# Performance work log

Hardware: AMD Instinct MI355X
Metric: run time of the kernel (lower is better)

Reference implementation:

```python
import jax, jax.numpy as jnp
import numpy as np

B, TK, NK, H = 64, 512, 256, 512

def _masked_renorm_softmax(scores, mask):
    # softmax over last dim, multiply by mask, renormalize (as in the torch code)
    p = jax.nn.softmax(scores, axis=-1) * mask
    return p / jnp.sum(p, axis=-1, keepdims=True)

def setup_inputs() -> dict:
    key = jax.random.key(0)
    ks = jax.random.split(key, 14)
    s = 0.02
    return {
        "s_t_hat": jax.random.normal(ks[0], (B, 2 * H), jnp.float32),
        "encoder_outputs_token": jax.random.normal(ks[1], (B, TK, H), jnp.float32),
        "encoder_outputs_node": jax.random.normal(ks[2], (B, NK, H), jnp.float32),
        "node_to_token": jax.random.randint(ks[3], (B, TK), 0, NK),
        "enc_padding_mask_token": jnp.ones((B, TK), jnp.float32),
        "enc_padding_mask_node": jnp.ones((B, NK), jnp.float32),
        "graph": jax.random.uniform(ks[4], (B, NK, NK), jnp.float32),
        "flow": jax.random.uniform(ks[5], (B, NK), jnp.float32),
        # parameters (Linear weights stored as [in, out]; x @ W == torch Linear)
        "W_c": jax.random.normal(ks[6], (H,), jnp.float32) * s,          # Linear(1, H)
        "W_tok": jax.random.normal(ks[7], (H, H), jnp.float32) * s,      # encode_proj_token
        "W_node": jax.random.normal(ks[8], (H, H), jnp.float32) * s,     # encode_proj_node
        "W_dec": jax.random.normal(ks[9], (2 * H, H), jnp.float32) * s,  # decode_proj
        "b_dec": jnp.zeros((H,), jnp.float32),
        "v_tok": jax.random.normal(ks[10], (H,), jnp.float32) * s,       # v_token
        "v_node": jax.random.normal(ks[11], (H,), jnp.float32) * s,      # v_node
    }

def reference(s_t_hat, encoder_outputs_token, encoder_outputs_node, node_to_token,
              enc_padding_mask_token, enc_padding_mask_node, graph, flow,
              W_c, W_tok, W_node, W_dec, b_dec, v_tok, v_node):
    # projections
    enc_tok_feat = jnp.einsum('bth,hk->btk', encoder_outputs_token, W_tok)   # [B,TK,H]
    enc_node_feat = jnp.einsum('bnh,hk->bnk', encoder_outputs_node, W_node)  # [B,NK,H]
    dec_fea = s_t_hat @ W_dec + b_dec                                        # [B,H]
    flow_feat = flow[..., None] * W_c                                        # [B,NK,H]

    # node attention
    e_node = jnp.tanh(enc_node_feat + dec_fea[:, None, :] + flow_feat)
    scores_node = jnp.einsum('bnh,h->bn', e_node, v_node)                    # [B,NK]
    attn_dist_node = _masked_renorm_softmax(scores_node, enc_padding_mask_node)

    # gather node attention onto tokens via node_to_token indices
    gathered = jnp.take_along_axis(attn_dist_node, node_to_token, axis=1)    # [B,TK]
    attn_dist_node_to_token = _masked_renorm_softmax(gathered, enc_padding_mask_token)

    # token attention
    e_tok = jnp.tanh(enc_tok_feat + dec_fea[:, None, :])
    scores_tok = jnp.einsum('bth,h->bt', e_tok, v_tok)                       # [B,TK]
    attn_dist_token = _masked_renorm_softmax(scores_tok, enc_padding_mask_token)

    # mix and context
    final_attn = 0.5 * attn_dist_token + 0.5 * attn_dist_node_to_token      # [B,TK]
    c_t = jnp.einsum('bt,bth->bh', final_attn, encoder_outputs_token)        # [B,H]

    # multi-hop graph diffusion of node attention
    zero_hop = attn_dist_node                                                # [B,NK]
    one_hop = jnp.einsum('bn,bnm->bm', zero_hop, graph)
    two_hop = jnp.einsum('bn,bnm->bm', one_hop, graph)
    flow_out = (zero_hop + one_hop + two_hop) * 0.33333

    return (c_t, final_attn, attn_dist_node, flow_out)
```

## Files before the change

kernel.cpp:

```cpp
#include <hip/hip_runtime.h>
#include <math.h>

constexpr int kB = 64;
constexpr int kTK = 512;
constexpr int kNK = 256;
constexpr int kH = 512;
constexpr int kTokBlocks = kB * kTK / 64;
constexpr int kNodeBlocks = kB * kNK / 64;

typedef float f32x4 __attribute__((ext_vector_type(4)));
typedef __bf16 bf16x8 __attribute__((ext_vector_type(8)));

__device__ __forceinline__ unsigned short f32_to_bf16(float f) {
  return (unsigned short)((__float_as_uint(f) + 0x8000u) >> 16);
}

__device__ __forceinline__ float tanh_fast(float x) {
  float e = __builtin_amdgcn_exp2f(x * 2.8853900817779268f);
  return 1.0f - 2.0f * __builtin_amdgcn_rcpf(e + 1.0f);
}

__device__ __forceinline__ void lds_barrier() {
  __builtin_amdgcn_s_waitcnt(0xC07F);
  __builtin_amdgcn_s_barrier();
}

__global__ __launch_bounds__(256) void prep_kernel(
    const float* __restrict__ Wtok, const float* __restrict__ Wnode,
    unsigned short* __restrict__ WtokT, unsigned short* __restrict__ WnodeT,
    const float* __restrict__ s_t_hat, const float* __restrict__ W_dec,
    float* __restrict__ dec_part) {
  __shared__ float sm[32 * 33];
  const int tid = threadIdx.x;
  if (blockIdx.x < 512) {
    const int idx = blockIdx.x;
    const int z = idx >> 8, rem = idx & 255;
    const int bx = rem & 15, by = rem >> 4;
    const float* W = z ? Wnode : Wtok;
    unsigned short* T = z ? WnodeT : WtokT;
    const int tx = tid & 31, ty = tid >> 5;
#pragma unroll
    for (int i = 0; i < 4; ++i)
      sm[(ty + 8 * i) * 33 + tx] =
          W[(size_t)(by * 32 + ty + 8 * i) * kH + bx * 32 + tx];
    __syncthreads();
#pragma unroll
    for (int i = 0; i < 4; ++i)
      T[(size_t)(bx * 32 + ty + 8 * i) * kH + by * 32 + tx] =
          f32_to_bf16(sm[tx * 33 + ty + 8 * i]);
  } else {
    const int r = blockIdx.x - 512;
    const int b = r >> 3, s = r & 7;
    if (tid < 128) sm[tid] = s_t_hat[(size_t)b * 1024 + s * 128 + tid];
    __syncthreads();
    float a0 = 0.f, a1 = 0.f;
    const float* w = W_dec + (size_t)(s * 128) * kH;
#pragma unroll 8
    for (int k = 0; k < 128; ++k) {
      a0 = fmaf(sm[k], w[(size_t)k * kH + tid], a0);
      a1 = fmaf(sm[k], w[(size_t)k * kH + tid + 256], a1);
    }
    dec_part[(size_t)(b * 8 + s) * kH + tid] = a0;
    dec_part[(size_t)(b * 8 + s) * kH + tid + 256] = a1;
  }
}

__global__ __launch_bounds__(1024, 4) void scores_fused_kernel(
    const float* __restrict__ enc_tok, const float* __restrict__ enc_node,
    const unsigned short* __restrict__ WtokT,
    const unsigned short* __restrict__ WnodeT,
    const float* __restrict__ dec_part, const float* __restrict__ b_dec,
    const float* __restrict__ flow, const float* __restrict__ W_c,
    const float* __restrict__ v_tok, const float* __restrict__ v_node,
    float* __restrict__ scores_tok, float* __restrict__ scores_node) {
  const int tid = threadIdx.x;
  const int wave = tid >> 6, lane = tid & 63;
  const int quad = lane >> 4, l15 = lane & 15;
  const bool is_node = blockIdx.x >= kTokBlocks;
  const int bidx = is_node ? (int)blockIdx.x - kTokBlocks : (int)blockIdx.x;
  const float* A = is_node ? enc_node : enc_tok;
  const unsigned short* WT = is_node ? WnodeT : WtokT;
  const float* v = is_node ? v_node : v_tok;
  float* scores = is_node ? scores_node : scores_tok;
  const int ROWS = is_node ? kNK : kTK;
  const int b = is_node ? (bidx >> 2) : (bidx >> 3);
  const int row0 = (is_node ? (bidx & 3) : (bidx & 7)) * 64;

  __shared__ __align__(16) unsigned short As[2][8192];
  __shared__ float red[16][64];

  const f32x4 fzero = {0.f, 0.f, 0.f, 0.f};
  f32x4 acc[4][2];
#pragma unroll
  for (int i = 0; i < 4; ++i)
#pragma unroll
    for (int j = 0; j < 2; ++j) acc[i][j] = fzero;

  const int r = tid >> 4;
  const int kcol = tid & 15;
  const float* aptr = A + (size_t)(b * ROWS + row0 + r) * kH + kcol * 4;
  const int k0 = kcol * 4;
  const int k1 = 64 + kcol * 4;
  const int addr0 = (((k0 >> 5) * 4 + (r >> 4)) * 64 + ((k0 >> 3) & 3) * 16 +
                     (r & 15)) * 8 + (k0 & 7);
  const int addr1 = (((k1 >> 5) * 4 + (r >> 4)) * 64 + ((k1 >> 3) & 3) * 16 +
                     (r & 15)) * 8 + (k1 & 7);
  float4 ax0, ax1;
  auto aload = [&](int kc) {
    ax0 = *(const float4*)(aptr + kc * 128);
    ax1 = *(const float4*)(aptr + kc * 128 + 64);
  };
  auto acommit = [&](int buf) {
    ushort4 h0, h1;
    h0.x = f32_to_bf16(ax0.x); h0.y = f32_to_bf16(ax0.y);
    h0.z = f32_to_bf16(ax0.z); h0.w = f32_to_bf16(ax0.w);
    h1.x = f32_to_bf16(ax1.x); h1.y = f32_to_bf16(ax1.y);
    h1.z = f32_to_bf16(ax1.z); h1.w = f32_to_bf16(ax1.w);
    *(ushort4*)&As[buf][addr0] = h0;
    *(ushort4*)&As[buf][addr1] = h1;
  };

  const int n0 = wave * 32;
  const unsigned short* bbase = WT + (size_t)(n0 + l15) * kH + quad * 8;
  bf16x8 bbuf[2][2];
  auto loadB = [&](int sb, int g) {
    bbuf[sb][0] = *(const bf16x8*)(bbase + g * 32);
    bbuf[sb][1] = *(const bf16x8*)(bbase + (size_t)16 * kH + g * 32);
  };

  aload(0);
  acommit(0);
  aload(1);
  loadB(0, 0);
  lds_barrier();

#pragma unroll
  for (int g = 0; g < 16; ++g) {
    const int kc = g >> 2, kh = g & 3;
    if (kh == 0 && kc < 3) {
      acommit((kc + 1) & 1);
      if (kc < 2) aload(kc + 2);
    }
    if (g < 15) loadB((g + 1) & 1, g + 1);
    bf16x8 afr[4];
#pragma unroll
    for (int mi = 0; mi < 4; ++mi)
      afr[mi] = *(const bf16x8*)&As[kc & 1][((kh * 4 + mi) * 64 + lane) * 8];
#pragma unroll
    for (int mi = 0; mi < 4; ++mi)
#pragma unroll
      for (int ni = 0; ni < 2; ++ni)
        acc[mi][ni] = __builtin_amdgcn_mfma_f32_16x16x32_bf16(
            afr[mi], bbuf[g & 1][ni], acc[mi][ni], 0, 0, 0);
    if (kh == 3 && kc < 3) lds_barrier();
  }

  float dec2[2], vv2[2], wc2[2];
#pragma unroll
  for (int ni = 0; ni < 2; ++ni) {
    const int col = n0 + 16 * ni + l15;
    float d = b_dec[col];
#pragma unroll
    for (int p = 0; p < 8; ++p) d += dec_part[(size_t)(b * 8 + p) * kH + col];
    dec2[ni] = d;
    vv2[ni] = v[col];
    wc2[ni] = is_node ? W_c[col] : 0.f;
  }
#pragma unroll
  for (int mi = 0; mi < 4; ++mi) {
#pragma unroll
    for (int reg = 0; reg < 4; ++reg) {
      const int row = 16 * mi + quad * 4 + reg;
      const float fl = is_node ? flow[b * kNK + row0 + row] : 0.f;
      float p = 0.f;
#pragma unroll
      for (int ni = 0; ni < 2; ++ni)
        p += tanh_fast(fmaf(fl, wc2[ni], acc[mi][ni][reg] + dec2[ni])) * vv2[ni];
#pragma unroll
      for (int off = 1; off < 16; off <<= 1) p += __shfl_xor(p, off, 64);
      if (l15 == 0) red[wave][row] = p;
    }
  }
  __syncthreads();
  if (tid < 64) {
    float s = 0.f;
#pragma unroll
    for (int w = 0; w < 16; ++w) s += red[w][tid];
    scores[b * ROWS + row0 + tid] = s;
  }
}

__device__ __forceinline__ float block_sum_512(float v, float* rbuf) {
#pragma unroll
  for (int off = 32; off >= 1; off >>= 1) v += __shfl_xor(v, off, 64);
  if ((threadIdx.x & 63) == 0) rbuf[threadIdx.x >> 6] = v;
  __syncthreads();
  float s = rbuf[0];
#pragma unroll
  for (int w = 1; w < 8; ++w) s += rbuf[w];
  __syncthreads();
  return s;
}

__global__ __launch_bounds__(512) void softmax_mix_kernel(
    const float* __restrict__ scores_node, const float* __restrict__ scores_tok,
    const int* __restrict__ node_to_token,
    const float* __restrict__ mask_tok, const float* __restrict__ mask_node,
    float* __restrict__ out_final, float* __restrict__ out_attn_node,
    float* __restrict__ out_flow) {
  const int b = blockIdx.x, tid = threadIdx.x;
  __shared__ float an_sh[kNK];
  __shared__ float rbuf[8];

  if (tid < kNK) out_flow[b * kNK + tid] = 0.f;

  float en = 0.f;
  if (tid < kNK)
    en = expf(scores_node[b * kNK + tid]) * mask_node[b * kNK + tid];
  float sn = block_sum_512(en, rbuf);
  float an = en / sn;
  if (tid < kNK) {
    an_sh[tid] = an;
    out_attn_node[b * kNK + tid] = an;
  }
  __syncthreads();

  const float mt = mask_tok[b * kTK + tid];
  const int idx = node_to_token[b * kTK + tid];
  float eg = expf(an_sh[idx]) * mt;
  float sg = block_sum_512(eg, rbuf);
  float an2t = eg / sg;

  float et = expf(scores_tok[b * kTK + tid]) * mt;
  float st = block_sum_512(et, rbuf);
  float at = et / st;

  out_final[b * kTK + tid] = 0.5f * (at + an2t);
}

__global__ __launch_bounds__(512) void ct_flow1_kernel(
    const float* __restrict__ final_attn, const float* __restrict__ enc_tok,
    const float* __restrict__ attn_node, const float* __restrict__ graph,
    float* __restrict__ ctp, float* __restrict__ fp1) {
  const int tid = threadIdx.x;
  if (blockIdx.x < 128) {
    const int b = blockIdx.x >> 1, s = blockIdx.x & 1;
    __shared__ float fa[256];
    if (tid < 256) fa[tid] = final_attn[b * kTK + s * 256 + tid];
    __syncthreads();
    const int h4 = (tid & 127) * 4, tsub = tid >> 7;
    float4 acc = {0.f, 0.f, 0.f, 0.f};
    const float* base =
        enc_tok + ((size_t)(b * kTK + s * 256 + tsub * 64)) * kH + h4;
#pragma unroll 8
    for (int t = 0; t < 64; ++t) {
      float4 e = *(const float4*)(base + (size_t)t * kH);
      const float w = fa[tsub * 64 + t];
      acc.x = fmaf(w, e.x, acc.x); acc.y = fmaf(w, e.y, acc.y);
      acc.z = fmaf(w, e.z, acc.z); acc.w = fmaf(w, e.w, acc.w);
    }
    *(float4*)&ctp[((size_t)(b * 8 + s * 4 + tsub)) * kH + h4] = acc;
  } else {
    const int rr = blockIdx.x - 128;
    const int b = rr >> 2, sl = rr & 3;
    __shared__ float z[64];
    __shared__ float part[8][256];
    if (tid < 64) z[tid] = attn_node[b * kNK + sl * 64 + tid];
    __syncthreads();
    const int m4 = (tid & 63) * 4, nsub = tid >> 6;
    float4 acc = {0.f, 0.f, 0.f, 0.f};
    const float* g =
        graph + ((size_t)(b * kNK + sl * 64 + nsub * 8)) * kNK + m4;
#pragma unroll
    for (int n = 0; n < 8; ++n) {
      float4 gg = *(const float4*)(g + (size_t)n * kNK);
      const float w = z[nsub * 8 + n];
      acc.x = fmaf(w, gg.x, acc.x); acc.y = fmaf(w, gg.y, acc.y);
      acc.z = fmaf(w, gg.z, acc.z); acc.w = fmaf(w, gg.w, acc.w);
    }
    *(float4*)&part[nsub][m4] = acc;
    __syncthreads();
    if (tid < 64) {
      float4 s0 = {0.f, 0.f, 0.f, 0.f};
#pragma unroll
      for (int p = 0; p < 8; ++p) {
        float4 pp = *(const float4*)&part[p][tid * 4];
        s0.x += pp.x; s0.y += pp.y; s0.z += pp.z; s0.w += pp.w;
      }
      *(float4*)&fp1[((size_t)(b * 4 + sl)) * kNK + tid * 4] = s0;
    }
  }
}

__global__ __launch_bounds__(512) void ct_flow2_kernel(
    const float* __restrict__ ctp, const float* __restrict__ fp1,
    const float* __restrict__ attn_node, const float* __restrict__ graph,
    float* __restrict__ out_ct, float* __restrict__ out_flow) {
  const int tid = threadIdx.x;
  if (blockIdx.x < 64) {
    const int b = blockIdx.x;
    __shared__ float acc_sh[4][512];
    const int h4 = (tid & 127) * 4, part = tid >> 7;
    float4 a = {0.f, 0.f, 0.f, 0.f};
#pragma unroll
    for (int j = 0; j < 2; ++j) {
      float4 c = *(const float4*)&ctp[((size_t)(b * 8 + part * 2 + j)) * kH + h4];
      a.x += c.x; a.y += c.y; a.z += c.z; a.w += c.w;
    }
    *(float4*)&acc_sh[part][h4] = a;
    __syncthreads();
    if (tid < 128) {
      float4 s = {0.f, 0.f, 0.f, 0.f};
#pragma unroll
      for (int p = 0; p < 4; ++p) {
        float4 pp = *(const float4*)&acc_sh[p][tid * 4];
        s.x += pp.x; s.y += pp.y; s.z += pp.z; s.w += pp.w;
      }
      *(float4*)&out_ct[b * kH + tid * 4] = s;
    }
  } else {
    const int rr = blockIdx.x - 64;
    const int b = rr >> 2, sl = rr & 3;
    __shared__ float one_sh[64];
    __shared__ float part2[8][256];
    if (tid < 64) {
      const int n = sl * 64 + tid;
      float one = 0.f;
#pragma unroll
      for (int p = 0; p < 4; ++p) one += fp1[((size_t)(b * 4 + p)) * kNK + n];
      one_sh[tid] = one;
      atomicAdd(&out_flow[b * kNK + n],
                (attn_node[b * kNK + n] + one) * 0.33333f);
    }
    __syncthreads();
    const int m4 = (tid & 63) * 4, nsub = tid >> 6;
    float4 acc = {0.f, 0.f, 0.f, 0.f};
    const float* g =
        graph + ((size_t)(b * kNK + sl * 64 + nsub * 8)) * kNK + m4;
#pragma unroll
    for (int n = 0; n < 8; ++n) {
      float4 gg = *(const float4*)(g + (size_t)n * kNK);
      const float w = one_sh[sl * 0 + nsub * 8 + n];
      acc.x = fmaf(w, gg.x, acc.x); acc.y = fmaf(w, gg.y, acc.y);
      acc.z = fmaf(w, gg.z, acc.z); acc.w = fmaf(w, gg.w, acc.w);
    }
    *(float4*)&part2[nsub][m4] = acc;
    __syncthreads();
    if (tid < 64) {
      float4 s = {0.f, 0.f, 0.f, 0.f};
#pragma unroll
      for (int p = 0; p < 8; ++p) {
        float4 pp = *(const float4*)&part2[p][tid * 4];
        s.x += pp.x; s.y += pp.y; s.z += pp.z; s.w += pp.w;
      }
      float* dst = &out_flow[b * kNK + tid * 4];
      atomicAdd(dst + 0, s.x * 0.33333f);
      atomicAdd(dst + 1, s.y * 0.33333f);
      atomicAdd(dst + 2, s.z * 0.33333f);
      atomicAdd(dst + 3, s.w * 0.33333f);
    }
  }
}

extern "C" void kernel_launch(void* const* d_in, const int* in_sizes, int n_in,
                              void* d_out, int out_size, void* d_ws, size_t ws_size,
                              hipStream_t stream) {
  (void)in_sizes; (void)n_in; (void)out_size; (void)ws_size;
  const float* s_t_hat  = (const float*)d_in[0];
  const float* enc_tok  = (const float*)d_in[1];
  const float* enc_node = (const float*)d_in[2];
  const int*   n2t      = (const int*)d_in[3];
  const float* mask_tok = (const float*)d_in[4];
  const float* mask_nd  = (const float*)d_in[5];
  const float* graph    = (const float*)d_in[6];
  const float* flow     = (const float*)d_in[7];
  const float* W_c      = (const float*)d_in[8];
  const float* W_tok    = (const float*)d_in[9];
  const float* W_node   = (const float*)d_in[10];
  const float* W_dec    = (const float*)d_in[11];
  const float* b_dec    = (const float*)d_in[12];
  const float* v_tok    = (const float*)d_in[13];
  const float* v_node   = (const float*)d_in[14];

  float* out = (float*)d_out;
  float* out_ct        = out;
  float* out_final     = out + kB * kH;
  float* out_attn_node = out + 2 * kB * kH;
  float* out_flow      = out_attn_node + kB * kNK;

  float* ws = (float*)d_ws;
  float* scores_tok  = ws;
  float* scores_node = ws + 32768;
  float* dec_part    = ws + 49152;
  float* ctp         = dec_part;
  float* fp1         = ws + 311296;
  unsigned short* WtokT  = (unsigned short*)(ws + 376832);
  unsigned short* WnodeT = WtokT + kH * kH;

  prep_kernel<<<1024, 256, 0, stream>>>(W_tok, W_node, WtokT, WnodeT,
                                        s_t_hat, W_dec, dec_part);
  scores_fused_kernel<<<kTokBlocks + kNodeBlocks, 1024, 0, stream>>>(
      enc_tok, enc_node, WtokT, WnodeT, dec_part, b_dec, flow, W_c,
      v_tok, v_node, scores_tok, scores_node);
  softmax_mix_kernel<<<kB, 512, 0, stream>>>(scores_node, scores_tok, n2t,
                                             mask_tok, mask_nd, out_final,
                                             out_attn_node, out_flow);
  ct_flow1_kernel<<<384, 512, 0, stream>>>(out_final, enc_tok, out_attn_node,
                                           graph, ctp, fp1);
  ct_flow2_kernel<<<320, 512, 0, stream>>>(ctp, fp1, out_attn_node, graph,
                                           out_ct, out_flow);
}
```

Baseline: 241.8 us.

## Retile scores GEMM to 128x128 blocks with async LDS B staging and atomics

Replaces the 1024-thread, 64-row by full-N scores kernel with 256-thread blocks computing 128x128 output tiles. The B operand is now staged into LDS through global_load_lds with an XOR swizzle instead of being loaded directly into registers. Because N is split across four column blocks, per-row partial scores are combined with atomicAdd, so prep_kernel now zeroes the score buffers. The larger tiles are meant to improve operand reuse and occupancy, at the cost of atomic contention and a single-buffered A/B pipeline with extra barriers.

Result: slower. 255.9 us (+5.8%).

```diff
diff --git a/kernel.cpp b/kernel.cpp
--- a/kernel.cpp
+++ b/kernel.cpp
@@ -5,11 +5,12 @@
 constexpr int kTK = 512;
 constexpr int kNK = 256;
 constexpr int kH = 512;
-constexpr int kTokBlocks = kB * kTK / 64;
-constexpr int kNodeBlocks = kB * kNK / 64;
+constexpr int kTokGemmBlocks = 256 * 4;
+constexpr int kNodeGemmBlocks = 128 * 4;
 
 typedef float f32x4 __attribute__((ext_vector_type(4)));
 typedef __bf16 bf16x8 __attribute__((ext_vector_type(8)));
+typedef unsigned short u16x8 __attribute__((ext_vector_type(8)));
 
 __device__ __forceinline__ unsigned short f32_to_bf16(float f) {
   return (unsigned short)((__float_as_uint(f) + 0x8000u) >> 16);
@@ -23,13 +24,19 @@
 __device__ __forceinline__ void lds_barrier() {
   __builtin_amdgcn_s_waitcnt(0xC07F);
   __builtin_amdgcn_s_barrier();
+}
+
+__device__ __forceinline__ void async_copy16(void* lds, const void* g) {
+  __builtin_amdgcn_global_load_lds(
+      (const __attribute__((address_space(1))) unsigned int*)g,
+      (__attribute__((address_space(3))) unsigned int*)lds, 16, 0, 0);
 }
 
 __global__ __launch_bounds__(256) void prep_kernel(
     const float* __restrict__ Wtok, const float* __restrict__ Wnode,
     unsigned short* __restrict__ WtokT, unsigned short* __restrict__ WnodeT,
     const float* __restrict__ s_t_hat, const float* __restrict__ W_dec,
-    float* __restrict__ dec_part) {
+    float* __restrict__ dec_part, float* __restrict__ scores_base) {
   __shared__ float sm[32 * 33];
   const int tid = threadIdx.x;
   if (blockIdx.x < 512) {
@@ -50,6 +57,8 @@
           f32_to_bf16(sm[tx * 33 + ty + 8 * i]);
   } else {
     const int r = blockIdx.x - 512;
+    const int tg = r * 256 + tid;
+    if (tg < kB * (kTK + kNK)) scores_base[tg] = 0.f;
     const int b = r >> 3, s = r & 7;
     if (tid < 128) sm[tid] = s_t_hat[(size_t)b * 1024 + s * 128 + tid];
     __syncthreads();
@@ -65,7 +74,7 @@
   }
 }
 
-__global__ __launch_bounds__(1024, 4) void scores_fused_kernel(
+__global__ __launch_bounds__(256, 3) void scores_mfma_kernel(
     const float* __restrict__ enc_tok, const float* __restrict__ enc_node,
     const unsigned short* __restrict__ WtokT,
     const unsigned short* __restrict__ WnodeT,
@@ -76,117 +85,128 @@
   const int tid = threadIdx.x;
   const int wave = tid >> 6, lane = tid & 63;
   const int quad = lane >> 4, l15 = lane & 15;
-  const bool is_node = blockIdx.x >= kTokBlocks;
-  const int bidx = is_node ? (int)blockIdx.x - kTokBlocks : (int)blockIdx.x;
+  const bool is_node = blockIdx.x >= kTokGemmBlocks;
+  const int idx = is_node ? (int)blockIdx.x - kTokGemmBlocks : (int)blockIdx.x;
+  const int rowblk = idx >> 2, colblk = idx & 3;
   const float* A = is_node ? enc_node : enc_tok;
   const unsigned short* WT = is_node ? WnodeT : WtokT;
   const float* v = is_node ? v_node : v_tok;
   float* scores = is_node ? scores_node : scores_tok;
-  const int ROWS = is_node ? kNK : kTK;
-  const int b = is_node ? (bidx >> 2) : (bidx >> 3);
-  const int row0 = (is_node ? (bidx & 3) : (bidx & 7)) * 64;
-
-  __shared__ __align__(16) unsigned short As[2][8192];
-  __shared__ float red[16][64];
+  const int grow0 = rowblk * 128;
+  const int bn = colblk * 128;
+
+  __shared__ __align__(16) unsigned short As[8192];
+  __shared__ __align__(16) unsigned short Bs[8192];
 
   const f32x4 fzero = {0.f, 0.f, 0.f, 0.f};
-  f32x4 acc[4][2];
+  f32x4 acc[4][4];
 #pragma unroll
   for (int i = 0; i < 4; ++i)
 #pragma unroll
-    for (int j = 0; j < 2; ++j) acc[i][j] = fzero;
-
-  const int r = tid >> 4;
-  const int kcol = tid & 15;
-  const float* aptr = A + (size_t)(b * ROWS + row0 + r) * kH + kcol * 4;
-  const int k0 = kcol * 4;
-  const int k1 = 64 + kcol * 4;
-  const int addr0 = (((k0 >> 5) * 4 + (r >> 4)) * 64 + ((k0 >> 3) & 3) * 16 +
-                     (r & 15)) * 8 + (k0 & 7);
-  const int addr1 = (((k1 >> 5) * 4 + (r >> 4)) * 64 + ((k1 >> 3) & 3) * 16 +
-                     (r & 15)) * 8 + (k1 & 7);
-  float4 ax0, ax1;
+    for (int j = 0; j < 4; ++j) acc[i][j] = fzero;
+
+  const int arow = tid >> 1, ahalf = tid & 1;
+  const float* aptr = A + (size_t)(grow0 + arow) * kH + ahalf * 32;
+  float4 ap[8];
   auto aload = [&](int kc) {
-    ax0 = *(const float4*)(aptr + kc * 128);
-    ax1 = *(const float4*)(aptr + kc * 128 + 64);
+#pragma unroll
+    for (int i = 0; i < 8; ++i)
+      ap[i] = *(const float4*)(aptr + kc * 64 + i * 4);
   };
-  auto acommit = [&](int buf) {
-    ushort4 h0, h1;
-    h0.x = f32_to_bf16(ax0.x); h0.y = f32_to_bf16(ax0.y);
-    h0.z = f32_to_bf16(ax0.z); h0.w = f32_to_bf16(ax0.w);
-    h1.x = f32_to_bf16(ax1.x); h1.y = f32_to_bf16(ax1.y);
-    h1.z = f32_to_bf16(ax1.z); h1.w = f32_to_bf16(ax1.w);
-    *(ushort4*)&As[buf][addr0] = h0;
-    *(ushort4*)&As[buf][addr1] = h1;
+  const int fbase = (ahalf * 8 + (arow >> 4)) * 512;
+  const int lbase = (arow & 15) * 8;
+  auto acommit = [&]() {
+#pragma unroll
+    for (int q2 = 0; q2 < 4; ++q2) {
+      u16x8 h;
+      h[0] = f32_to_bf16(ap[q2 * 2].x); h[1] = f32_to_bf16(ap[q2 * 2].y);
+      h[2] = f32_to_bf16(ap[q2 * 2].z); h[3] = f32_to_bf16(ap[q2 * 2].w);
+      h[4] = f32_to_bf16(ap[q2 * 2 + 1].x); h[5] = f32_to_bf16(ap[q2 * 2 + 1].y);
+      h[6] = f32_to_bf16(ap[q2 * 2 + 1].z); h[7] = f32_to_bf16(ap[q2 * 2 + 1].w);
+      *(u16x8*)&As[fbase + q2 * 128 + lbase] = h;
+    }
   };
 
-  const int n0 = wave * 32;
-  const unsigned short* bbase = WT + (size_t)(n0 + l15) * kH + quad * 8;
-  bf16x8 bbuf[2][2];
-  auto loadB = [&](int sb, int g) {
-    bbuf[sb][0] = *(const bf16x8*)(bbase + g * 32);
-    bbuf[sb][1] = *(const bf16x8*)(bbase + (size_t)16 * kH + g * 32);
+  const int nr8 = tid >> 3, kslot = tid & 7;
+  auto stageB = [&](int kc) {
+#pragma unroll
+    for (int j = 0; j < 4; ++j) {
+      const int nrow = j * 32 + nr8;
+      const unsigned short* g =
+          WT + (size_t)(bn + nrow) * kH + kc * 64 + ((kslot ^ (nrow & 7)) * 8);
+      async_copy16(&Bs[j * 2048 + wave * 512], g);
+    }
   };
 
+  const int wm = (wave >> 1) * 4;
+  const int wn = (wave & 1) * 64;
+  auto compute = [&]() {
+#pragma unroll
+    for (int kh = 0; kh < 2; ++kh) {
+      bf16x8 afr[4], bfr[4];
+#pragma unroll
+      for (int mi = 0; mi < 4; ++mi)
+        afr[mi] = *(const bf16x8*)&As[(kh * 8 + wm + mi) * 512 + lane * 8];
+#pragma unroll
+      for (int ni = 0; ni < 4; ++ni) {
+        const int nl = wn + ni * 16 + l15;
+        const int s = kh * 4 + quad;
+        bfr[ni] = *(const bf16x8*)&Bs[nl * 64 + ((s ^ (nl & 7)) * 8)];
+      }
+#pragma unroll
+      for (int mi = 0; mi < 4; ++mi)
+#pragma unroll
+        for (int ni = 0; ni < 4; ++ni)
+          acc[mi][ni] = __builtin_amdgcn_mfma_f32_16x16x32_bf16(
+              afr[mi], bfr[ni], acc[mi][ni], 0, 0, 0);
+    }
+  };
+
   aload(0);
-  acommit(0);
+  acommit();
+  stageB(0);
   aload(1);
-  loadB(0, 0);
-  lds_barrier();
-
-#pragma unroll
-  for (int g = 0; g < 16; ++g) {
-    const int kc = g >> 2, kh = g & 3;
-    if (kh == 0 && kc < 3) {
-      acommit((kc + 1) & 1);
-      if (kc < 2) aload(kc + 2);
-    }
-    if (g < 15) loadB((g + 1) & 1, g + 1);
-    bf16x8 afr[4];
-#pragma unroll
-    for (int mi = 0; mi < 4; ++mi)
-      afr[mi] = *(const bf16x8*)&As[kc & 1][((kh * 4 + mi) * 64 + lane) * 8];
-#pragma unroll
-    for (int mi = 0; mi < 4; ++mi)
-#pragma unroll
-      for (int ni = 0; ni < 2; ++ni)
-        acc[mi][ni] = __builtin_amdgcn_mfma_f32_16x16x32_bf16(
-            afr[mi], bbuf[g & 1][ni], acc[mi][ni], 0, 0, 0);
-    if (kh == 3 && kc < 3) lds_barrier();
-  }
-
-  float dec2[2], vv2[2], wc2[2];
-#pragma unroll
-  for (int ni = 0; ni < 2; ++ni) {
-    const int col = n0 + 16 * ni + l15;
+  __syncthreads();
+
+#pragma unroll 1
+  for (int kc = 0; kc < 8; ++kc) {
+    compute();
+    if (kc < 7) {
+      lds_barrier();
+      acommit();
+      stageB(kc + 1);
+      if (kc < 6) aload(kc + 2);
+      __syncthreads();
+    }
+  }
+
+  const int bb = is_node ? (grow0 >> 8) : (grow0 >> 9);
+  float dec4[4], vv4[4], wc4[4];
+#pragma unroll
+  for (int ni = 0; ni < 4; ++ni) {
+    const int col = bn + wn + ni * 16 + l15;
     float d = b_dec[col];
 #pragma unroll
-    for (int p = 0; p < 8; ++p) d += dec_part[(size_t)(b * 8 + p) * kH + col];
-    dec2[ni] = d;
-    vv2[ni] = v[col];
-    wc2[ni] = is_node ? W_c[col] : 0.f;
-  }
+    for (int p = 0; p < 8; ++p) d += dec_part[(size_t)(bb * 8 + p) * kH + col];
+    dec4[ni] = d;
+    vv4[ni] = v[col];
+    wc4[ni] = is_node ? W_c[col] : 0.f;
+  }
+  const int rbase = grow0 + (wave >> 1) * 64;
 #pragma unroll
   for (int mi = 0; mi < 4; ++mi) {
 #pragma unroll
     for (int reg = 0; reg < 4; ++reg) {
-      const int row = 16 * mi + quad * 4 + reg;
-      const float fl = is_node ? flow[b * kNK + row0 + row] : 0.f;
+      const int row = rbase + 16 * mi + quad * 4 + reg;
+      const float fl = is_node ? flow[row] : 0.f;
       float p = 0.f;
 #pragma unroll
-      for (int ni = 0; ni < 2; ++ni)
-        p += tanh_fast(fmaf(fl, wc2[ni], acc[mi][ni][reg] + dec2[ni])) * vv2[ni];
+      for (int ni = 0; ni < 4; ++ni)
+        p += tanh_fast(fmaf(fl, wc4[ni], acc[mi][ni][reg] + dec4[ni])) * vv4[ni];
 #pragma unroll
       for (int off = 1; off < 16; off <<= 1) p += __shfl_xor(p, off, 64);
-      if (l15 == 0) red[wave][row] = p;
-    }
-  }
-  __syncthreads();
-  if (tid < 64) {
-    float s = 0.f;
-#pragma unroll
-    for (int w = 0; w < 16; ++w) s += red[w][tid];
-    scores[b * ROWS + row0 + tid] = s;
+      if (l15 == 0) atomicAdd(&scores[row], p);
+    }
   }
 }
 
@@ -340,7 +360,7 @@
 #pragma unroll
     for (int n = 0; n < 8; ++n) {
       float4 gg = *(const float4*)(g + (size_t)n * kNK);
-      const float w = one_sh[sl * 0 + nsub * 8 + n];
+      const float w = one_sh[nsub * 8 + n];
       acc.x = fmaf(w, gg.x, acc.x); acc.y = fmaf(w, gg.y, acc.y);
       acc.z = fmaf(w, gg.z, acc.z); acc.w = fmaf(w, gg.w, acc.w);
     }
@@ -398,8 +418,8 @@
   unsigned short* WnodeT = WtokT + kH * kH;
 
   prep_kernel<<<1024, 256, 0, stream>>>(W_tok, W_node, WtokT, WnodeT,
-                                        s_t_hat, W_dec, dec_part);
-  scores_fused_kernel<<<kTokBlocks + kNodeBlocks, 1024, 0, stream>>>(
+                                        s_t_hat, W_dec, dec_part, scores_tok);
+  scores_mfma_kernel<<<kTokGemmBlocks + kNodeGemmBlocks, 256, 0, stream>>>(
       enc_tok, enc_node, WtokT, WnodeT, dec_part, b_dec, flow, W_c,
       v_tok, v_node, scores_tok, scores_node);
   softmax_mix_kernel<<<kB, 512, 0, stream>>>(scores_node, scores_tok, n2t,
```
